# Performance work log

Hardware: AMD Instinct MI355X
Metric: run time of the kernel (lower is better)

The kernel has to match this reference:

```python
import jax, jax.numpy as jnp
import numpy as np

# --- config constants (from init_kwargs) ---
ALPHA = 0.05; SIGMA = 0.2; THETA = 0.3; A = 0.02; B_PAR = 0.1; RHO = 0.5
MULT = 2.0          # config.x_range_final[1]
GAMMA = 0.5         # power-utility exponent: u(x,r)=r*x^g/g, ux=r*x^(g-1)
N_STEPS = 100; T_FINAL = 1.0; DT = T_FINAL / N_STEPS
HID = 64; BATCH = 16384
PEN_SCALE = 100.0; LOWER = 1e-6


def _mlp(W1, b1, W2, b2, W3, b3, s):
    # tiny FeedForwardSubNet: 3 -> HID -> HID -> 1, tanh activations
    h = jnp.tanh(s @ W1 + b1)
    h = jnp.tanh(h @ W2 + b2)
    return h @ W3 + b3


def _penalise(v):
    # penalise_range(v, lower): quadratic hinge below `lower`
    return PEN_SCALE * jnp.square(jnp.maximum(LOWER - v, 0.0))


def setup_inputs() -> dict:
    key = jax.random.key(0)
    ks = jax.random.split(key, 16)
    dw = jax.random.normal(ks[0], (BATCH, 1, N_STEPS), dtype=jnp.float32) * float(np.sqrt(DT))
    X0 = jnp.ones((1,), jnp.float32)
    R0 = jnp.ones((1,), jnp.float32)
    def w(k, shape, fan):
        return jax.random.normal(k, shape, jnp.float32) / np.float32(np.sqrt(fan))
    inp = {"dw": dw, "X0": X0, "R0": R0,
           "pW1": w(ks[1], (3, HID), 3), "pb1": jnp.zeros((HID,), jnp.float32),
           "pW2": w(ks[2], (HID, HID), HID), "pb2": jnp.zeros((HID,), jnp.float32),
           "pW3": w(ks[3], (HID, 1), HID), "pb3": jnp.zeros((1,), jnp.float32),
           "qW1": w(ks[4], (3, HID), 3), "qb1": jnp.zeros((HID,), jnp.float32),
           "qW2": w(ks[5], (HID, HID), HID), "qb2": jnp.zeros((HID,), jnp.float32),
           "qW3": w(ks[6], (HID, 1), HID), "qb3": jnp.zeros((1,), jnp.float32)}
    return inp


def reference(dw, X0, R0, pW1, pb1, pW2, pb2, pW3, pb3, qW1, qb1, qW2, qb2, qW3, qb3):
    Bn = dw.shape[0]
    ones = jnp.ones((Bn, 1), dw.dtype)
    times = jnp.arange(N_STEPS + 1, dtype=dw.dtype) * DT   # [N+1]
    x0 = ones * X0
    R0v = ones * R0
    b_eff = float(np.sign(RHO)) * B_PAR

    # p_0 and dp_0 = d p_0 / d x (per-sample, rowwise independent net)
    def p_of_x(xx):
        st = jnp.concatenate([MULT * times[0] * ones, xx, R0v], 1)
        return _mlp(pW1, pb1, pW2, pb2, pW3, pb3, st)
    p0, p_vjp = jax.vjp(p_of_x, x0)
    (dp0,) = p_vjp(jnp.ones_like(p0))
    pi0 = _mlp(qW1, qb1, qW2, qb2, qW3, qb3,
               jnp.concatenate([MULT * times[0] * ones, x0, R0v], 1))

    dw_t = jnp.transpose(dw, (2, 0, 1))          # [N, B, 1]
    upd = jnp.arange(N_STEPS) < (N_STEPS - 1)    # pi not updated at last step

    def step(carry, inp):
        x, min_x, W, pi = carry
        dwi, t_next, u = inp
        x = x + x * ALPHA * DT + pi * SIGMA * THETA * DT + pi * SIGMA * dwi
        min_x = jnp.minimum(x, min_x)
        W = W + dwi
        Rv = R0v * jnp.exp((A - 0.5 * b_eff ** 2) * t_next + b_eff * W)
        p = p0 * jnp.exp(-(ALPHA + 0.5 * THETA ** 2) * t_next - THETA * W)
        st = jnp.concatenate([MULT * t_next * jnp.ones_like(x), x, Rv], 1)
        pi_new = _mlp(qW1, qb1, qW2, qb2, qW3, qb3, st)
        pi = jnp.where(u, pi_new, pi)
        return (x, min_x, W, pi), (x, Rv, pi, -p)

    (xf, min_x, Wf, pif), (xs, Rs, pis, dMs) = jax.lax.scan(
        step, (x0, x0, jnp.zeros_like(x0), pi0), (dw_t, times[1:], upd))

    # stacked process data, matching tf.concat-over-axis-0 ordering: [(N+1)*B, 1]
    x_all  = jnp.concatenate([x0[None], xs], 0).reshape(-1, 1)
    r_all  = jnp.concatenate([R0v[None], Rs], 0).reshape(-1, 1)
    pi_all = jnp.concatenate([pi0[None], pis], 0).reshape(-1, 1)
    dM_all = jnp.concatenate([(-p0)[None], dMs], 0).reshape(-1, 1)
    dM2_all = jnp.tile(-dp0, (N_STEPS + 1, 1))
    proc = jnp.concatenate([x_all, r_all, pi_all, dM_all, dM2_all], 1)  # [(N+1)*B, 5]

    # losses (non_concave = False branch)
    p_fin = -dMs[-1]
    R_fin = Rs[-1]
    xc = jnp.maximum(xf, LOWER)
    ux = R_fin * xc ** (GAMMA - 1.0)
    u_val = R_fin * xc ** GAMMA / GAMMA
    pen = _penalise(min_x)
    loss_p = jnp.mean(jnp.square(p_fin + ux) + pen)
    loss_pi = loss_p + jnp.mean(-u_val + pen)

    return jnp.concatenate([proc.reshape(-1), jnp.stack([loss_p, loss_pi])])
```

## Files before the change

kernel.cpp:

```cpp
#include <hip/hip_runtime.h>
#include <math.h>

#define NSTEP 100
#define BATCH 16384
#define MB 32
#define NBLK (BATCH/MB)
#define NT 256

#define C_ALPHA 0.05f
#define C_SIGMA 0.2f
#define C_THETA 0.3f
#define C_DT    0.01f
#define C_LOWER 1e-6f
#define C_PEN   100.0f
#define RV_T  0.015f
#define RV_W  0.1f
#define P_T  (-0.095f)
#define P_W  (-0.3f)

typedef __attribute__((ext_vector_type(8))) short bf16x8;
typedef __attribute__((ext_vector_type(4))) float f32x4;

__device__ __forceinline__ float fast_tanh(float x) {
    float e = __builtin_amdgcn_exp2f(x * 2.885390082f);
    return 1.0f - 2.0f * __builtin_amdgcn_rcpf(e + 1.0f);
}
__device__ __forceinline__ unsigned short f2bf(float f) {
    unsigned u = __float_as_uint(f);
    return (unsigned short)((u + 0x7FFFu + ((u >> 16) & 1u)) >> 16);
}

__global__ void init_kernel(const float* X0, const float* R0,
                            const float* pW1, const float* pb1, const float* pW2,
                            const float* pb2, const float* pW3, const float* pb3,
                            const float* qW1, const float* qb1, const float* qW2,
                            const float* qb2, const float* qW3, const float* qb3,
                            float* ws) {
    __shared__ float lh[64], ld[64];
    int j = threadIdx.x;
    float sx = X0[0], sr = R0[0];
    {
        float pre = pW1[64 + j] * sx + pW1[128 + j] * sr + pb1[j];
        float h1 = fast_tanh(pre);
        float d1 = (1.0f - h1 * h1) * pW1[64 + j];
        lh[j] = h1; ld[j] = d1;
        __syncthreads();
        float pre2 = pb2[j], dpre2 = 0.0f;
        for (int i = 0; i < 64; i++) {
            float w = pW2[i * 64 + j];
            pre2 += lh[i] * w;
            dpre2 += ld[i] * w;
        }
        float h2 = fast_tanh(pre2);
        float d2 = (1.0f - h2 * h2) * dpre2;
        float c1 = h2 * pW3[j], c2 = d2 * pW3[j];
        for (int o = 32; o >= 1; o >>= 1) {
            c1 += __shfl_down(c1, o);
            c2 += __shfl_down(c2, o);
        }
        if (j == 0) { ws[0] = c1 + pb3[0]; ws[1] = c2; }
        __syncthreads();
    }
    {
        float pre = qW1[64 + j] * sx + qW1[128 + j] * sr + qb1[j];
        float h1 = fast_tanh(pre);
        lh[j] = h1;
        __syncthreads();
        float pre2 = qb2[j];
        for (int i = 0; i < 64; i++) pre2 += lh[i] * qW2[i * 64 + j];
        float h2 = fast_tanh(pre2);
        float c1 = h2 * qW3[j];
        for (int o = 32; o >= 1; o >>= 1) c1 += __shfl_down(c1, o);
        if (j == 0) { ws[2] = c1 + qb3[0]; ws[3] = 0.0f; ws[4] = 0.0f; }
    }
}

__global__ __launch_bounds__(NT, 2) void step_kernel(
        const float* __restrict__ dw, const float* __restrict__ X0,
        const float* __restrict__ R0,
        const float* __restrict__ qW1, const float* __restrict__ qb1,
        const float* __restrict__ qW2, const float* __restrict__ qb2,
        const float* __restrict__ qW3, const float* __restrict__ qb3,
        float* __restrict__ ws, float* __restrict__ out) {
    __shared__ __align__(16) unsigned short sW2T[64 * 72];
    __shared__ __align__(16) unsigned short sH1[MB * 72];
    __shared__ float sx[MB], sr[MB];
    __shared__ __align__(16) float sP[2][MB];

    const int tid = threadIdx.x;
    const int b0 = blockIdx.x * MB;
    const int lane = tid & 63;
    const int wv = tid >> 6;
    const int mt = wv & 1;
    const int nh = wv >> 1;
    const int l15 = lane & 15, quad = lane >> 4;

    for (int u = tid; u < 64 * 64; u += NT) {
        int k = u >> 6, n = u & 63;
        sW2T[n * 72 + k] = f2bf(qW2[u]);
    }
    const int jj = tid & 63;
    const int mg = tid >> 6;
    const float w1t = qW1[jj], w1x = qW1[64 + jj], w1r = qW1[128 + jj], b1 = qb1[jj];
    const int n0 = nh * 32 + l15;
    const int n1 = n0 + 16;
    const float b2v0 = qb2[n0], b2v1 = qb2[n1];
    const float w3v0 = qW3[n0], w3v1 = qW3[n1];
    const float b3 = qb3[0];
    const float p0 = ws[0], dp0 = ws[1], pi0 = ws[2];
    __syncthreads();

    bf16x8 Bf00 = *(const bf16x8*)&sW2T[n0 * 72 + quad * 8];
    bf16x8 Bf10 = *(const bf16x8*)&sW2T[n0 * 72 + 32 + quad * 8];
    bf16x8 Bf01 = *(const bf16x8*)&sW2T[n1 * 72 + quad * 8];
    bf16x8 Bf11 = *(const bf16x8*)&sW2T[n1 * 72 + 32 + quad * 8];

    const bool own = (tid < MB);
    float x = 0.f, Wsum = 0.f, minx = 0.f, R0v = 0.f, pi = 0.f;
    if (own) {
        x = X0[0]; R0v = R0[0]; minx = x; pi = pi0;
        size_t base = (size_t)(b0 + tid) * 5;
        out[base] = x; out[base + 1] = R0v; out[base + 2] = pi0;
        out[base + 3] = -p0; out[base + 4] = -dp0;
    }

    #pragma unroll 1
    for (int i = 0; i < NSTEP - 1; i++) {
        if (own) {
            int m = tid;
            if (i > 0) {
                pi = sP[0][m] + sP[1][m] + b3;
                out[((size_t)i * BATCH + b0 + m) * 5 + 2] = pi;
            }
            float dwv = dw[(size_t)(b0 + m) * NSTEP + i];
            x = x * (1.0f + C_ALPHA * C_DT) + pi * C_SIGMA * (C_THETA * C_DT + dwv);
            minx = fminf(minx, x);
            Wsum += dwv;
            float tn = C_DT * (float)(i + 1);
            float Rv = R0v * __expf(RV_T * tn + RV_W * Wsum);
            float pm = p0 * __expf(P_T * tn + P_W * Wsum);
            sx[m] = x; sr[m] = Rv;
            size_t base = ((size_t)(i + 1) * BATCH + b0 + m) * 5;
            out[base] = x; out[base + 1] = Rv;
            out[base + 3] = -pm; out[base + 4] = -dp0;
        }
        __syncthreads();

        {
            float c0 = w1t * (2.0f * C_DT * (float)(i + 1)) + b1;
            #pragma unroll
            for (int mm = 0; mm < 8; mm++) {
                int m = mg * 8 + mm;
                float h = fast_tanh(c0 + w1x * sx[m] + w1r * sr[m]);
                sH1[m * 72 + jj] = f2bf(h);
            }
        }
        __syncthreads();

        const unsigned short* arow = &sH1[(mt * 16 + l15) * 72 + quad * 8];
        bf16x8 A0 = *(const bf16x8*)arow;
        bf16x8 A1 = *(const bf16x8*)(arow + 32);
        f32x4 acc0 = {b2v0, b2v0, b2v0, b2v0};
        f32x4 acc1 = {b2v1, b2v1, b2v1, b2v1};
        acc0 = __builtin_amdgcn_mfma_f32_16x16x32_bf16(A0, Bf00, acc0, 0, 0, 0);
        acc0 = __builtin_amdgcn_mfma_f32_16x16x32_bf16(A1, Bf10, acc0, 0, 0, 0);
        acc1 = __builtin_amdgcn_mfma_f32_16x16x32_bf16(A0, Bf01, acc1, 0, 0, 0);
        acc1 = __builtin_amdgcn_mfma_f32_16x16x32_bf16(A1, Bf11, acc1, 0, 0, 0);
        f32x4 part;
        #pragma unroll
        for (int r = 0; r < 4; r++)
            part[r] = fast_tanh(acc0[r]) * w3v0 + fast_tanh(acc1[r]) * w3v1;
        #pragma unroll
        for (int o = 1; o < 16; o <<= 1) {
            part[0] += __shfl_xor(part[0], o);
            part[1] += __shfl_xor(part[1], o);
            part[2] += __shfl_xor(part[2], o);
            part[3] += __shfl_xor(part[3], o);
        }
        if (l15 == 0)
            *(f32x4*)&sP[nh][mt * 16 + quad * 4] = part;
        __syncthreads();
    }

    if (own) {
        int m = tid;
        pi = sP[0][m] + sP[1][m] + b3;
        out[((size_t)(NSTEP - 1) * BATCH + b0 + m) * 5 + 2] = pi;
        float dwv = dw[(size_t)(b0 + m) * NSTEP + (NSTEP - 1)];
        x = x * (1.0f + C_ALPHA * C_DT) + pi * C_SIGMA * (C_THETA * C_DT + dwv);
        minx = fminf(minx, x);
        Wsum += dwv;
        float Rf = R0v * __expf(RV_T * 1.0f + RV_W * Wsum);
        float pf = p0 * __expf(P_T * 1.0f + P_W * Wsum);
        size_t base = ((size_t)NSTEP * BATCH + b0 + m) * 5;
        out[base] = x; out[base + 1] = Rf; out[base + 2] = pi;
        out[base + 3] = -pf; out[base + 4] = -dp0;

        float xc = fmaxf(x, C_LOWER);
        float ux = Rf * rsqrtf(xc);
        float uval = 2.0f * Rf * sqrtf(xc);
        float d = fmaxf(C_LOWER - minx, 0.0f);
        float pen = C_PEN * d * d;
        float t1 = pf + ux;
        float v1 = t1 * t1 + pen;
        float v2 = -uval + pen;
        #pragma unroll
        for (int o = 16; o >= 1; o >>= 1) {
            v1 += __shfl_down(v1, o);
            v2 += __shfl_down(v2, o);
        }
        if (tid == 0) {
            atomicAdd(&ws[3], v1);
            atomicAdd(&ws[4], v2);
        }
    }
}

__global__ void fin_kernel(const float* ws, float* out) {
    float lp = ws[3] * (1.0f / (float)BATCH);
    float lq = ws[4] * (1.0f / (float)BATCH);
    out[(size_t)(NSTEP + 1) * BATCH * 5] = lp;
    out[(size_t)(NSTEP + 1) * BATCH * 5 + 1] = lp + lq;
}

extern "C" void kernel_launch(void* const* d_in, const int* in_sizes, int n_in,
                              void* d_out, int out_size, void* d_ws, size_t ws_size,
                              hipStream_t stream) {
    const float* dw  = (const float*)d_in[0];
    const float* X0  = (const float*)d_in[1];
    const float* R0  = (const float*)d_in[2];
    const float* pW1 = (const float*)d_in[3];
    const float* pb1 = (const float*)d_in[4];
    const float* pW2 = (const float*)d_in[5];
    const float* pb2 = (const float*)d_in[6];
    const float* pW3 = (const float*)d_in[7];
    const float* pb3 = (const float*)d_in[8];
    const float* qW1 = (const float*)d_in[9];
    const float* qb1 = (const float*)d_in[10];
    const float* qW2 = (const float*)d_in[11];
    const float* qb2 = (const float*)d_in[12];
    const float* qW3 = (const float*)d_in[13];
    const float* qb3 = (const float*)d_in[14];
    float* out = (float*)d_out;
    float* ws  = (float*)d_ws;

    init_kernel<<<1, 64, 0, stream>>>(X0, R0, pW1, pb1, pW2, pb2, pW3, pb3,
                                      qW1, qb1, qW2, qb2, qW3, qb3, ws);
    step_kernel<<<NBLK, NT, 0, stream>>>(dw, X0, R0, qW1, qb1, qW2, qb2, qW3, qb3,
                                         ws, out);
    fin_kernel<<<1, 1, 0, stream>>>(ws, out);
}
```

Baseline: 233.5 us.

## Restructure step kernel to single-wave blocks with register-resident layer-1 and fused finalize

Each block now holds 16 samples and a single 64-lane wavefront. This removes every per-step __syncthreads, and layer-1 activations are computed directly into MFMA A-fragment registers instead of going through shared memory. The dw slice is preloaded into LDS, and the tanh input scaling is folded into the weights and biases. The separate finalize kernel is replaced by a last-block atomic counter, and the init kernel now stages weights in LDS and uses shuffles. The trade-offs are twice as many blocks, four MFMA n-tiles per wave with redundant layer-1 work per lane, and a dependency on ws[5] being zeroed by the init kernel.

```diff
diff --git a/kernel.cpp b/kernel.cpp
--- a/kernel.cpp
+++ b/kernel.cpp
@@ -3,9 +3,9 @@
 
 #define NSTEP 100
 #define BATCH 16384
-#define MB 32
+#define MB 16
 #define NBLK (BATCH/MB)
-#define NT 256
+#define NT 64
 
 #define C_ALPHA 0.05f
 #define C_SIGMA 0.2f
@@ -13,21 +13,23 @@
 #define C_DT    0.01f
 #define C_LOWER 1e-6f
 #define C_PEN   100.0f
-#define RV_T  0.015f
-#define RV_W  0.1f
-#define P_T  (-0.095f)
-#define P_W  (-0.3f)
+#define LOG2E   1.4426950408889634f
+#define TSCALE  (2.0f * LOG2E)
+#define CRT ( 0.015f * C_DT * LOG2E)
+#define CRW ( 0.1f * LOG2E)
+#define CPT (-0.095f * C_DT * LOG2E)
+#define CPW (-0.3f * LOG2E)
 
 typedef __attribute__((ext_vector_type(8))) short bf16x8;
 typedef __attribute__((ext_vector_type(4))) float f32x4;
 
-__device__ __forceinline__ float fast_tanh(float x) {
-    float e = __builtin_amdgcn_exp2f(x * 2.885390082f);
+__device__ __forceinline__ float tanh_pre(float zs) {
+    float e = __builtin_amdgcn_exp2f(zs);
     return 1.0f - 2.0f * __builtin_amdgcn_rcpf(e + 1.0f);
 }
-__device__ __forceinline__ unsigned short f2bf(float f) {
+__device__ __forceinline__ unsigned f2bf_u(float f) {
     unsigned u = __float_as_uint(f);
-    return (unsigned short)((u + 0x7FFFu + ((u >> 16) & 1u)) >> 16);
+    return (u + 0x7FFFu + ((u >> 16) & 1u)) >> 16;
 }
 
 __global__ void init_kernel(const float* X0, const float* R0,
@@ -36,46 +38,44 @@
                             const float* qW1, const float* qb1, const float* qW2,
                             const float* qb2, const float* qW3, const float* qb3,
                             float* ws) {
-    __shared__ float lh[64], ld[64];
-    int j = threadIdx.x;
+    __shared__ float sw[2][4096];
+    int tid = threadIdx.x;
+    for (int u = tid; u < 4096; u += 256) { sw[0][u] = pW2[u]; sw[1][u] = qW2[u]; }
+    __syncthreads();
+    int wv = tid >> 6, j = tid & 63;
     float sx = X0[0], sr = R0[0];
-    {
+    if (wv == 0) {
         float pre = pW1[64 + j] * sx + pW1[128 + j] * sr + pb1[j];
-        float h1 = fast_tanh(pre);
+        float h1 = tanh_pre(TSCALE * pre);
         float d1 = (1.0f - h1 * h1) * pW1[64 + j];
-        lh[j] = h1; ld[j] = d1;
-        __syncthreads();
         float pre2 = pb2[j], dpre2 = 0.0f;
-        for (int i = 0; i < 64; i++) {
-            float w = pW2[i * 64 + j];
-            pre2 += lh[i] * w;
-            dpre2 += ld[i] * w;
-        }
-        float h2 = fast_tanh(pre2);
+        #pragma unroll 8
+        for (int i2 = 0; i2 < 64; i2++) {
+            float w = sw[0][i2 * 64 + j];
+            pre2  += __shfl(h1, i2) * w;
+            dpre2 += __shfl(d1, i2) * w;
+        }
+        float h2 = tanh_pre(TSCALE * pre2);
         float d2 = (1.0f - h2 * h2) * dpre2;
         float c1 = h2 * pW3[j], c2 = d2 * pW3[j];
         for (int o = 32; o >= 1; o >>= 1) {
-            c1 += __shfl_down(c1, o);
-            c2 += __shfl_down(c2, o);
+            c1 += __shfl_down(c1, o); c2 += __shfl_down(c2, o);
         }
         if (j == 0) { ws[0] = c1 + pb3[0]; ws[1] = c2; }
-        __syncthreads();
-    }
-    {
+    } else if (wv == 1) {
         float pre = qW1[64 + j] * sx + qW1[128 + j] * sr + qb1[j];
-        float h1 = fast_tanh(pre);
-        lh[j] = h1;
-        __syncthreads();
+        float h1 = tanh_pre(TSCALE * pre);
         float pre2 = qb2[j];
-        for (int i = 0; i < 64; i++) pre2 += lh[i] * qW2[i * 64 + j];
-        float h2 = fast_tanh(pre2);
+        #pragma unroll 8
+        for (int i2 = 0; i2 < 64; i2++) pre2 += __shfl(h1, i2) * sw[1][i2 * 64 + j];
+        float h2 = tanh_pre(TSCALE * pre2);
         float c1 = h2 * qW3[j];
         for (int o = 32; o >= 1; o >>= 1) c1 += __shfl_down(c1, o);
-        if (j == 0) { ws[2] = c1 + qb3[0]; ws[3] = 0.0f; ws[4] = 0.0f; }
-    }
-}
-
-__global__ __launch_bounds__(NT, 2) void step_kernel(
+        if (j == 0) { ws[2] = c1 + qb3[0]; ws[3] = 0.0f; ws[4] = 0.0f; ws[5] = 0.0f; }
+    }
+}
+
+__global__ __launch_bounds__(NT, 1) void step_kernel(
         const float* __restrict__ dw, const float* __restrict__ X0,
         const float* __restrict__ R0,
         const float* __restrict__ qW1, const float* __restrict__ qb1,
@@ -83,93 +83,111 @@
         const float* __restrict__ qW3, const float* __restrict__ qb3,
         float* __restrict__ ws, float* __restrict__ out) {
     __shared__ __align__(16) unsigned short sW2T[64 * 72];
-    __shared__ __align__(16) unsigned short sH1[MB * 72];
-    __shared__ float sx[MB], sr[MB];
-    __shared__ __align__(16) float sP[2][MB];
-
-    const int tid = threadIdx.x;
+    __shared__ __align__(16) float sdw[MB * NSTEP];
+    __shared__ __align__(16) float sPi[MB];
+
+    const int lane = threadIdx.x;
     const int b0 = blockIdx.x * MB;
-    const int lane = tid & 63;
-    const int wv = tid >> 6;
-    const int mt = wv & 1;
-    const int nh = wv >> 1;
     const int l15 = lane & 15, quad = lane >> 4;
 
-    for (int u = tid; u < 64 * 64; u += NT) {
-        int k = u >> 6, n = u & 63;
-        sW2T[n * 72 + k] = f2bf(qW2[u]);
-    }
-    const int jj = tid & 63;
-    const int mg = tid >> 6;
-    const float w1t = qW1[jj], w1x = qW1[64 + jj], w1r = qW1[128 + jj], b1 = qb1[jj];
-    const int n0 = nh * 32 + l15;
-    const int n1 = n0 + 16;
-    const float b2v0 = qb2[n0], b2v1 = qb2[n1];
-    const float w3v0 = qW3[n0], w3v1 = qW3[n1];
+    {
+        const float4* g = (const float4*)(dw + (size_t)b0 * NSTEP);
+        float4* s = (float4*)sdw;
+        #pragma unroll
+        for (int u = lane; u < MB * NSTEP / 4; u += NT) s[u] = g[u];
+    }
+    #pragma unroll 8
+    for (int t = 0; t < 64; t++) {
+        float w = qW2[t * 64 + lane];
+        sW2T[lane * 72 + t] = (unsigned short)f2bf_u(w * TSCALE);
+    }
+    bf16x8 Bf[4][2];
+    #pragma unroll
+    for (int nt = 0; nt < 4; nt++) {
+        const unsigned short* r = &sW2T[(nt * 16 + l15) * 72 + quad * 8];
+        Bf[nt][0] = *(const bf16x8*)r;
+        Bf[nt][1] = *(const bf16x8*)(r + 32);
+    }
+    float tco[16], w1xs[16], w1rs[16], b1s[16];
+    #pragma unroll
+    for (int idx = 0; idx < 16; idx++) {
+        int k = (idx < 8) ? (quad * 8 + idx) : (32 + quad * 8 + (idx - 8));
+        tco[idx]  = qW1[k] * (2.0f * C_DT * TSCALE);
+        w1xs[idx] = qW1[64 + k] * TSCALE;
+        w1rs[idx] = qW1[128 + k] * TSCALE;
+        b1s[idx]  = qb1[k] * TSCALE;
+    }
+    float b2v[4], w3v[4];
+    #pragma unroll
+    for (int nt = 0; nt < 4; nt++) {
+        b2v[nt] = qb2[nt * 16 + l15] * TSCALE;
+        w3v[nt] = qW3[nt * 16 + l15];
+    }
     const float b3 = qb3[0];
     const float p0 = ws[0], dp0 = ws[1], pi0 = ws[2];
-    __syncthreads();
-
-    bf16x8 Bf00 = *(const bf16x8*)&sW2T[n0 * 72 + quad * 8];
-    bf16x8 Bf10 = *(const bf16x8*)&sW2T[n0 * 72 + 32 + quad * 8];
-    bf16x8 Bf01 = *(const bf16x8*)&sW2T[n1 * 72 + quad * 8];
-    bf16x8 Bf11 = *(const bf16x8*)&sW2T[n1 * 72 + 32 + quad * 8];
-
-    const bool own = (tid < MB);
+    const float X0v = X0[0], R0s = R0[0];
+
     float x = 0.f, Wsum = 0.f, minx = 0.f, R0v = 0.f, pi = 0.f;
-    if (own) {
-        x = X0[0]; R0v = R0[0]; minx = x; pi = pi0;
-        size_t base = (size_t)(b0 + tid) * 5;
+    float v1 = 0.f, v2 = 0.f;
+    if (lane < MB) {
+        x = X0v; R0v = R0s; minx = x; pi = pi0;
+        sPi[lane] = pi0;
+        size_t base = (size_t)(b0 + lane) * 5;
         out[base] = x; out[base + 1] = R0v; out[base + 2] = pi0;
         out[base + 3] = -p0; out[base + 4] = -dp0;
     }
 
     #pragma unroll 1
     for (int i = 0; i < NSTEP - 1; i++) {
-        if (own) {
-            int m = tid;
-            if (i > 0) {
-                pi = sP[0][m] + sP[1][m] + b3;
-                out[((size_t)i * BATCH + b0 + m) * 5 + 2] = pi;
-            }
-            float dwv = dw[(size_t)(b0 + m) * NSTEP + i];
+        float fi = (float)(i + 1);
+        float Rcur = 0.f;
+        if (lane < MB) {
+            pi = sPi[lane];
+            float dwv = sdw[lane * NSTEP + i];
             x = x * (1.0f + C_ALPHA * C_DT) + pi * C_SIGMA * (C_THETA * C_DT + dwv);
             minx = fminf(minx, x);
             Wsum += dwv;
-            float tn = C_DT * (float)(i + 1);
-            float Rv = R0v * __expf(RV_T * tn + RV_W * Wsum);
-            float pm = p0 * __expf(P_T * tn + P_W * Wsum);
-            sx[m] = x; sr[m] = Rv;
-            size_t base = ((size_t)(i + 1) * BATCH + b0 + m) * 5;
-            out[base] = x; out[base + 1] = Rv;
+            Rcur = R0v * __builtin_amdgcn_exp2f(fmaf(CRW, Wsum, CRT * fi));
+            float pm = p0 * __builtin_amdgcn_exp2f(fmaf(CPW, Wsum, CPT * fi));
+            size_t base = ((size_t)(i + 1) * BATCH + b0 + lane) * 5;
+            out[base] = x; out[base + 1] = Rcur;
             out[base + 3] = -pm; out[base + 4] = -dp0;
         }
-        __syncthreads();
-
+        float xb = __shfl(x, l15);
+        float rb = __shfl(Rcur, l15);
+
+        union { bf16x8 v; unsigned u[4]; } A0, A1;
+        #pragma unroll
+        for (int p = 0; p < 8; p++) {
+            int i0 = 2 * p, i1 = 2 * p + 1;
+            float z0 = fmaf(w1rs[i0], rb, fmaf(w1xs[i0], xb, fmaf(tco[i0], fi, b1s[i0])));
+            float z1 = fmaf(w1rs[i1], rb, fmaf(w1xs[i1], xb, fmaf(tco[i1], fi, b1s[i1])));
+            unsigned pk = f2bf_u(tanh_pre(z0)) | (f2bf_u(tanh_pre(z1)) << 16);
+            if (p < 4) A0.u[p] = pk; else A1.u[p - 4] = pk;
+        }
+        f32x4 part;
         {
-            float c0 = w1t * (2.0f * C_DT * (float)(i + 1)) + b1;
+            f32x4 acc0 = {b2v[0], b2v[0], b2v[0], b2v[0]};
+            f32x4 acc1 = {b2v[1], b2v[1], b2v[1], b2v[1]};
+            f32x4 acc2 = {b2v[2], b2v[2], b2v[2], b2v[2]};
+            f32x4 acc3 = {b2v[3], b2v[3], b2v[3], b2v[3]};
+            acc0 = __builtin_amdgcn_mfma_f32_16x16x32_bf16(A0.v, Bf[0][0], acc0, 0, 0, 0);
+            acc1 = __builtin_amdgcn_mfma_f32_16x16x32_bf16(A0.v, Bf[1][0], acc1, 0, 0, 0);
+            acc2 = __builtin_amdgcn_mfma_f32_16x16x32_bf16(A0.v, Bf[2][0], acc2, 0, 0, 0);
+            acc3 = __builtin_amdgcn_mfma_f32_16x16x32_bf16(A0.v, Bf[3][0], acc3, 0, 0, 0);
+            acc0 = __builtin_amdgcn_mfma_f32_16x16x32_bf16(A1.v, Bf[0][1], acc0, 0, 0, 0);
+            acc1 = __builtin_amdgcn_mfma_f32_16x16x32_bf16(A1.v, Bf[1][1], acc1, 0, 0, 0);
+            acc2 = __builtin_amdgcn_mfma_f32_16x16x32_bf16(A1.v, Bf[2][1], acc2, 0, 0, 0);
+            acc3 = __builtin_amdgcn_mfma_f32_16x16x32_bf16(A1.v, Bf[3][1], acc3, 0, 0, 0);
             #pragma unroll
-            for (int mm = 0; mm < 8; mm++) {
-                int m = mg * 8 + mm;
-                float h = fast_tanh(c0 + w1x * sx[m] + w1r * sr[m]);
-                sH1[m * 72 + jj] = f2bf(h);
+            for (int r = 0; r < 4; r++) {
+                float s = tanh_pre(acc0[r]) * w3v[0];
+                s = fmaf(tanh_pre(acc1[r]), w3v[1], s);
+                s = fmaf(tanh_pre(acc2[r]), w3v[2], s);
+                s = fmaf(tanh_pre(acc3[r]), w3v[3], s);
+                part[r] = s;
             }
         }
-        __syncthreads();
-
-        const unsigned short* arow = &sH1[(mt * 16 + l15) * 72 + quad * 8];
-        bf16x8 A0 = *(const bf16x8*)arow;
-        bf16x8 A1 = *(const bf16x8*)(arow + 32);
-        f32x4 acc0 = {b2v0, b2v0, b2v0, b2v0};
-        f32x4 acc1 = {b2v1, b2v1, b2v1, b2v1};
-        acc0 = __builtin_amdgcn_mfma_f32_16x16x32_bf16(A0, Bf00, acc0, 0, 0, 0);
-        acc0 = __builtin_amdgcn_mfma_f32_16x16x32_bf16(A1, Bf10, acc0, 0, 0, 0);
-        acc1 = __builtin_amdgcn_mfma_f32_16x16x32_bf16(A0, Bf01, acc1, 0, 0, 0);
-        acc1 = __builtin_amdgcn_mfma_f32_16x16x32_bf16(A1, Bf11, acc1, 0, 0, 0);
-        f32x4 part;
-        #pragma unroll
-        for (int r = 0; r < 4; r++)
-            part[r] = fast_tanh(acc0[r]) * w3v0 + fast_tanh(acc1[r]) * w3v1;
         #pragma unroll
         for (int o = 1; o < 16; o <<= 1) {
             part[0] += __shfl_xor(part[0], o);
@@ -177,22 +195,25 @@
             part[2] += __shfl_xor(part[2], o);
             part[3] += __shfl_xor(part[3], o);
         }
-        if (l15 == 0)
-            *(f32x4*)&sP[nh][mt * 16 + quad * 4] = part;
-        __syncthreads();
-    }
-
-    if (own) {
-        int m = tid;
-        pi = sP[0][m] + sP[1][m] + b3;
-        out[((size_t)(NSTEP - 1) * BATCH + b0 + m) * 5 + 2] = pi;
-        float dwv = dw[(size_t)(b0 + m) * NSTEP + (NSTEP - 1)];
+        if (l15 == 0) {
+            float q0 = part[0] + b3, q1 = part[1] + b3;
+            float q2 = part[2] + b3, q3 = part[3] + b3;
+            f32x4 pv = {q0, q1, q2, q3};
+            *(f32x4*)&sPi[quad * 4] = pv;
+            size_t base = ((size_t)(i + 1) * BATCH + b0 + quad * 4) * 5 + 2;
+            out[base] = q0; out[base + 5] = q1; out[base + 10] = q2; out[base + 15] = q3;
+        }
+    }
+
+    if (lane < MB) {
+        pi = sPi[lane];
+        float dwv = sdw[lane * NSTEP + (NSTEP - 1)];
         x = x * (1.0f + C_ALPHA * C_DT) + pi * C_SIGMA * (C_THETA * C_DT + dwv);
         minx = fminf(minx, x);
         Wsum += dwv;
-        float Rf = R0v * __expf(RV_T * 1.0f + RV_W * Wsum);
-        float pf = p0 * __expf(P_T * 1.0f + P_W * Wsum);
-        size_t base = ((size_t)NSTEP * BATCH + b0 + m) * 5;
+        float Rf = R0v * __builtin_amdgcn_exp2f(fmaf(CRW, Wsum, CRT * (float)NSTEP));
+        float pf = p0 * __builtin_amdgcn_exp2f(fmaf(CPW, Wsum, CPT * (float)NSTEP));
+        size_t base = ((size_t)NSTEP * BATCH + b0 + lane) * 5;
         out[base] = x; out[base + 1] = Rf; out[base + 2] = pi;
         out[base + 3] = -pf; out[base + 4] = -dp0;
 
@@ -202,25 +223,26 @@
         float d = fmaxf(C_LOWER - minx, 0.0f);
         float pen = C_PEN * d * d;
         float t1 = pf + ux;
-        float v1 = t1 * t1 + pen;
-        float v2 = -uval + pen;
-        #pragma unroll
-        for (int o = 16; o >= 1; o >>= 1) {
-            v1 += __shfl_down(v1, o);
-            v2 += __shfl_down(v2, o);
-        }
-        if (tid == 0) {
-            atomicAdd(&ws[3], v1);
-            atomicAdd(&ws[4], v2);
-        }
-    }
-}
-
-__global__ void fin_kernel(const float* ws, float* out) {
-    float lp = ws[3] * (1.0f / (float)BATCH);
-    float lq = ws[4] * (1.0f / (float)BATCH);
-    out[(size_t)(NSTEP + 1) * BATCH * 5] = lp;
-    out[(size_t)(NSTEP + 1) * BATCH * 5 + 1] = lp + lq;
+        v1 = t1 * t1 + pen;
+        v2 = -uval + pen;
+    }
+    #pragma unroll
+    for (int o = 8; o >= 1; o >>= 1) {
+        v1 += __shfl_down(v1, o);
+        v2 += __shfl_down(v2, o);
+    }
+    if (lane == 0) {
+        atomicAdd(&ws[3], v1);
+        atomicAdd(&ws[4], v2);
+        __threadfence();
+        int old = atomicAdd((int*)(ws + 5), 1);
+        if (old == NBLK - 1) {
+            float lp = atomicAdd(&ws[3], 0.0f) * (1.0f / (float)BATCH);
+            float lq = atomicAdd(&ws[4], 0.0f) * (1.0f / (float)BATCH);
+            out[(size_t)(NSTEP + 1) * BATCH * 5] = lp;
+            out[(size_t)(NSTEP + 1) * BATCH * 5 + 1] = lp + lq;
+        }
+    }
 }
 
 extern "C" void kernel_launch(void* const* d_in, const int* in_sizes, int n_in,
@@ -244,9 +266,8 @@
     float* out = (float*)d_out;
     float* ws  = (float*)d_ws;
 
-    init_kernel<<<1, 64, 0, stream>>>(X0, R0, pW1, pb1, pW2, pb2, pW3, pb3,
-                                      qW1, qb1, qW2, qb2, qW3, qb3, ws);
+    init_kernel<<<1, 256, 0, stream>>>(X0, R0, pW1, pb1, pW2, pb2, pW3, pb3,
+                                       qW1, qb1, qW2, qb2, qW3, qb3, ws);
     step_kernel<<<NBLK, NT, 0, stream>>>(dw, X0, R0, qW1, qb1, qW2, qb2, qW3, qb3,
                                          ws, out);
-    fin_kernel<<<1, 1, 0, stream>>>(ws, out);
-}
+}
```

After: 229.0 us. Within noise of the previous version (-1.9%).
